# Optimization experiments

Hardware: AMD Instinct MI355X
Metric: run time of the kernel (lower is better)

## Reference

```python
import jax, jax.numpy as jnp
import numpy as np

B, L, D_MODEL = 2, 1024, 512
N_LAYERS, D_STATE, D_CONV = 6, 16, 4
D_INNER = 2 * D_MODEL          # Mamba default expand=2
DT_RANK = (D_MODEL + 15) // 16  # ceil(d_model/16) = 32
EPS = 1.1920929e-07             # torch RMSNorm default eps (fp32 machine eps)


def rmsnorm(x, w):
    return x * jax.lax.rsqrt(jnp.mean(x * x, axis=-1, keepdims=True) + EPS) * w


def selective_scan(u, dt, A, Bm, Cm, Dv):
    # u, dt: (B,L,E); A: (E,N); Bm, Cm: (B,L,N); Dv: (E,)
    dA = jnp.exp(jnp.einsum('ble,en->blen', dt, A))    # discretized A (ZOH)
    dBu = jnp.einsum('ble,bln->blen', dt * u, Bm)      # discretized B * u (Euler)

    def step(h, inp):
        dA_t, dBu_t, C_t = inp
        h = dA_t * h + dBu_t                           # (B,E,N) state update
        y = jnp.einsum('ben,bn->be', h, C_t)
        return h, y

    h0 = jnp.zeros((u.shape[0], u.shape[2], A.shape[1]), u.dtype)
    _, ys = jax.lax.scan(step, h0,
                         (dA.transpose(1, 0, 2, 3), dBu.transpose(1, 0, 2, 3),
                          Cm.transpose(1, 0, 2)))
    return ys.transpose(1, 0, 2) + u * Dv


def mamba_block(x, p):
    xz = jnp.einsum('bld,ed->ble', x, p['in_proj_w'])  # (B,L,2E)
    xi, z = jnp.split(xz, 2, axis=-1)
    # causal depthwise conv1d (kernel D_CONV) + bias + SiLU
    xc = jnp.pad(xi.transpose(0, 2, 1), ((0, 0), (0, 0), (D_CONV - 1, 0)))
    xc = jax.lax.conv_general_dilated(xc, p['conv_w'][:, None, :], (1,), 'VALID',
                                      feature_group_count=D_INNER)
    xi = jax.nn.silu(xc.transpose(0, 2, 1) + p['conv_b'])
    dbc = jnp.einsum('ble,re->blr', xi, p['x_proj_w'])  # (B,L,R+2N)
    dt, Bm, Cm = jnp.split(dbc, [DT_RANK, DT_RANK + D_STATE], axis=-1)
    dt = jax.nn.softplus(jnp.einsum('blr,er->ble', dt, p['dt_w']) + p['dt_b'])
    y = selective_scan(xi, dt, -jnp.exp(p['A_log']), Bm, Cm, p['D'])
    y = y * jax.nn.silu(z)                              # gate branch
    return jnp.einsum('ble,de->bld', y, p['out_w'])


def setup_inputs() -> dict:
    key = jax.random.key(0)
    ks = jax.random.split(key, 8)
    s = 0.02
    return {
        'x': jax.random.normal(ks[0], (B, L, D_MODEL), jnp.float32),
        'position_embedding': jax.random.normal(ks[1], (B, L, D_MODEL), jnp.float32) * 0.02,
        'norm_w': jnp.ones((D_MODEL,), jnp.float32),
        'in_proj_w': jax.random.normal(ks[2], (N_LAYERS, 2 * D_INNER, D_MODEL), jnp.float32) * s,
        'conv_w': jax.random.normal(ks[3], (N_LAYERS, D_INNER, D_CONV), jnp.float32) * 0.2,
        'conv_b': jnp.zeros((N_LAYERS, D_INNER), jnp.float32),
        'x_proj_w': jax.random.normal(ks[4], (N_LAYERS, DT_RANK + 2 * D_STATE, D_INNER), jnp.float32) * s,
        'dt_w': jax.random.normal(ks[5], (N_LAYERS, D_INNER, DT_RANK), jnp.float32) * s,
        'dt_b': jnp.full((N_LAYERS, D_INNER), -4.6, jnp.float32),  # softplus(dt_b) ~ 0.01
        'A_log': jnp.broadcast_to(
            jnp.log(jnp.arange(1, D_STATE + 1, dtype=jnp.float32)),
            (N_LAYERS, D_INNER, D_STATE)) + jnp.zeros((N_LAYERS, D_INNER, D_STATE), jnp.float32),
        'D': jnp.ones((N_LAYERS, D_INNER), jnp.float32),
        'out_w': jax.random.normal(ks[6], (N_LAYERS, D_MODEL, D_INNER), jnp.float32) * s,
    }


def reference(x, position_embedding, norm_w, in_proj_w, conv_w, conv_b,
              x_proj_w, dt_w, dt_b, A_log, D, out_w):
    stacked = dict(in_proj_w=in_proj_w, conv_w=conv_w, conv_b=conv_b,
                   x_proj_w=x_proj_w, dt_w=dt_w, dt_b=dt_b,
                   A_log=A_log, D=D, out_w=out_w)

    def body(h, p):
        h = h + position_embedding          # added at the start of every layer
        h = mamba_block(rmsnorm(h, norm_w), p)  # NOTE: no residual, per source
        return h, None

    h, _ = jax.lax.scan(body, x, stacked)
    return h
```

## Files before the change

kernel.cpp:

```cpp
#include <hip/hip_runtime.h>
#include <hip/hip_bf16.h>


typedef __attribute__((ext_vector_type(8))) short bf16x8;
typedef __attribute__((ext_vector_type(4))) float f32x4;

__device__ __forceinline__ float bf2f(unsigned short u) {
    unsigned int x = ((unsigned int)u) << 16;
    return __builtin_bit_cast(float, x);
}
__device__ __forceinline__ unsigned short f2bf(float f) {
    __hip_bfloat16 h = __float2bfloat16(f);
    return __builtin_bit_cast(unsigned short, h);
}
__device__ __forceinline__ float ldin(const void* p, size_t i, int isbf) {
    return isbf ? bf2f(((const unsigned short*)p)[i]) : ((const float*)p)[i];
}
__device__ __forceinline__ float softplus_f(float x) {
    return (x > 20.f) ? x : log1pf(__expf(x));
}
__device__ __forceinline__ void split2(float x, unsigned short& h, unsigned short& l) {
    h = f2bf(x);
    l = f2bf(x - bf2f(h));
}

#define S1 (6*2048*512)
#define S2 (6*512*1024)
#define S3 (6*64*1024)
#define S4 (6*1024*32)
#define S5 (6*1024*16)
#define S6 (6*4*1024)
#define S7 (6*1024)
__global__ __launch_bounds__(256) void wsplit_all(
    const void* __restrict__ ipw, const void* __restrict__ ow,
    const void* __restrict__ xpw, const void* __restrict__ dtw,
    const void* __restrict__ alog, const void* __restrict__ cw,
    const void* __restrict__ cb, const void* __restrict__ Dw,
    unsigned short* __restrict__ h1, unsigned short* __restrict__ l1,
    unsigned short* __restrict__ h2, unsigned short* __restrict__ l2,
    unsigned short* __restrict__ h3, unsigned short* __restrict__ l3,
    float* __restrict__ dtwT, float* __restrict__ AenT,
    float* __restrict__ cwT, float* __restrict__ cbF,
    int* __restrict__ flag)
{
    int g = blockIdx.x * 256 + threadIdx.x;
    const int isbf = (*(const unsigned int*)Dw == 0x3F800000u) ? 0 : 1;
    if (g == 0) *flag = isbf;
    if (g < S1 + S2 + S3) {
        const void* src; unsigned short *dh, *dl; int i;
        if (g < S1)            { src = ipw; dh = h1; dl = l1; i = g; }
        else if (g < S1 + S2)  { src = ow;  dh = h2; dl = l2; i = g - S1; }
        else                   { src = xpw; dh = h3; dl = l3; i = g - S1 - S2; }
        unsigned short hh, ll;
        split2(ldin(src, i, isbf), hh, ll);
        dh[i] = hh; dl[i] = ll;
    } else if (g < S1 + S2 + S3 + S4) {
        int i = g - (S1 + S2 + S3);
        int l = i >> 15, rem = i & 32767;
        int e = rem >> 5, k = rem & 31;
        dtwT[(size_t)l * 32768 + k * 1024 + e] =
            ldin(dtw, (size_t)l * 32768 + e * 32 + k, isbf);
    } else if (g < S1 + S2 + S3 + S4 + S5) {
        int i = g - (S1 + S2 + S3 + S4);
        int l = i >> 14, rem = i & 16383;
        int n = rem >> 10, e = rem & 1023;
        AenT[(size_t)l * 16384 + n * 1024 + e] =
            -__expf(ldin(alog, (size_t)l * 16384 + e * 16 + n, isbf));
    } else if (g < S1 + S2 + S3 + S4 + S5 + S6) {
        int i = g - (S1 + S2 + S3 + S4 + S5);
        int l = i >> 12, rem = i & 4095;
        int k = rem >> 10, e = rem & 1023;
        cwT[(size_t)l * 4096 + k * 1024 + e] =
            ldin(cw, (size_t)l * 4096 + e * 4 + k, isbf);
    } else if (g < S1 + S2 + S3 + S4 + S5 + S6 + S7) {
        int i = g - (S1 + S2 + S3 + S4 + S5 + S6);
        cbF[i] = ldin(cb, i, isbf);
    }
}

__global__ __launch_bounds__(512) void gemm128(
    const unsigned short* __restrict__ Ah, const unsigned short* __restrict__ Al,
    int lda,
    const unsigned short* __restrict__ Wh, const unsigned short* __restrict__ Wl,
    long woff,
    float* __restrict__ Cf, int N, int K)
{
    __shared__ __align__(16) unsigned short As[2][128][40];
    __shared__ __align__(16) unsigned short Ws[2][128][40];

    const int bid = blockIdx.x;
    const int xcd = bid & 7, s = bid >> 3;
    const int mt = (xcd >> 1) * 4 + (s & 3);
    const int nt = (xcd & 1) * 8 + (s >> 2);
    const int m0 = mt * 128, n0 = nt * 128;

    const int t = threadIdx.x, lane = t & 63, wave = t >> 6;
    const int wm = (wave & 1) * 64, wn = (wave >> 1) * 32;
    const int srow = t >> 2, scol = (t & 3) * 8;

    const unsigned short* ah = Ah + (size_t)(m0 + srow) * lda + scol;
    const unsigned short* al = Al + (size_t)(m0 + srow) * lda + scol;
    const unsigned short* wh = Wh + woff + (size_t)(n0 + srow) * K + scol;
    const unsigned short* wl = Wl + woff + (size_t)(n0 + srow) * K + scol;

    f32x4 acc[4][2] = {};
    const int fm = lane & 15, fk = (lane >> 4) * 8;

    uint4 r0, r1, r2, r3;
#define LD128(K0) do { \
        r0 = *(const uint4*)(ah + (K0)); \
        r1 = *(const uint4*)(al + (K0)); \
        r2 = *(const uint4*)(wh + (K0)); \
        r3 = *(const uint4*)(wl + (K0)); \
    } while (0)
#define ST128() do { \
        *(uint4*)(&As[0][srow][scol]) = r0; \
        *(uint4*)(&As[1][srow][scol]) = r1; \
        *(uint4*)(&Ws[0][srow][scol]) = r2; \
        *(uint4*)(&Ws[1][srow][scol]) = r3; \
    } while (0)

    LD128(0);
    ST128();
    __syncthreads();

    for (int k0 = 0; k0 < K; k0 += 32) {
        const int more = (k0 + 32 < K);
        if (more) LD128(k0 + 32);

        bf16x8 a_h[4], a_l[4], w_h[2], w_l[2];
#pragma unroll
        for (int i = 0; i < 4; ++i) {
            a_h[i] = *(const bf16x8*)(&As[0][wm + i * 16 + fm][fk]);
            a_l[i] = *(const bf16x8*)(&As[1][wm + i * 16 + fm][fk]);
        }
#pragma unroll
        for (int j = 0; j < 2; ++j) {
            w_h[j] = *(const bf16x8*)(&Ws[0][wn + j * 16 + fm][fk]);
            w_l[j] = *(const bf16x8*)(&Ws[1][wn + j * 16 + fm][fk]);
        }
#pragma unroll
        for (int mi = 0; mi < 4; ++mi)
#pragma unroll
            for (int ni = 0; ni < 2; ++ni) {
                acc[mi][ni] = __builtin_amdgcn_mfma_f32_16x16x32_bf16(
                    a_h[mi], w_h[ni], acc[mi][ni], 0, 0, 0);
                acc[mi][ni] = __builtin_amdgcn_mfma_f32_16x16x32_bf16(
                    a_h[mi], w_l[ni], acc[mi][ni], 0, 0, 0);
                acc[mi][ni] = __builtin_amdgcn_mfma_f32_16x16x32_bf16(
                    a_l[mi], w_h[ni], acc[mi][ni], 0, 0, 0);
            }

        if (more) {
            __syncthreads();
            ST128();
            __syncthreads();
        }
    }
#undef LD128
#undef ST128

    const int col = lane & 15, rb = (lane >> 4) * 4;
#pragma unroll
    for (int mi = 0; mi < 4; ++mi)
#pragma unroll
        for (int ni = 0; ni < 2; ++ni)
#pragma unroll
            for (int r = 0; r < 4; ++r) {
                int gm = m0 + wm + mi * 16 + rb + r;
                int gn = n0 + wn + ni * 16 + col;
                Cf[(size_t)gm * N + gn] = acc[mi][ni][r];
            }
}

template <int ACT, int SWZ>
__global__ __launch_bounds__(512) void gemm_hl(
    const unsigned short* __restrict__ Ah, const unsigned short* __restrict__ Al,
    int lda,
    const unsigned short* __restrict__ Wh, const unsigned short* __restrict__ Wl,
    long woff,
    float* __restrict__ Cf, long zstride,
    const void* __restrict__ bias, long boff, const int* __restrict__ flag,
    int N, int K, int Kc)
{
    const int isbf = *flag;
    __shared__ __align__(16) unsigned short As[2][2][64][40];
    __shared__ __align__(16) unsigned short Ws[2][2][64][40];

    int m0, n0, kb;
    if (SWZ) {
        const int bid = blockIdx.x;
        const int xcd = bid & 7, s = bid >> 3;
        m0 = (xcd * 4 + (s & 3)) * 64;
        n0 = (s >> 2) * 64;
        kb = 0;
    } else {
        m0 = blockIdx.x * 64; n0 = blockIdx.y * 64; kb = blockIdx.z * Kc;
    }
    const int t = threadIdx.x;
    const int lane = t & 63, wave = t >> 6;
    const int wm = (wave & 1) * 32, wn = (wave >> 1) * 16;
    const int u = t & 255;
    const int srow = u >> 2, scol = (u & 3) * 8;
    const int isA = (t < 256);

    const unsigned short* ph = isA ? (Ah + (size_t)(m0 + srow) * lda + scol)
                                   : (Wh + woff + (size_t)(n0 + srow) * K + scol);
    const unsigned short* pl = isA ? (Al + (size_t)(m0 + srow) * lda + scol)
                                   : (Wl + woff + (size_t)(n0 + srow) * K + scol);

    f32x4 acc[2] = {};

    uint4 r0, r1;
#define LD64(K0) do { \
        r0 = *(const uint4*)(ph + (K0)); \
        r1 = *(const uint4*)(pl + (K0)); \
    } while (0)
#define ST64(B) do { \
        if (isA) { \
            *(uint4*)(&As[B][0][srow][scol]) = r0; \
            *(uint4*)(&As[B][1][srow][scol]) = r1; \
        } else { \
            *(uint4*)(&Ws[B][0][srow][scol]) = r0; \
            *(uint4*)(&Ws[B][1][srow][scol]) = r1; \
        } \
    } while (0)

    LD64(kb);
    ST64(0);
    __syncthreads();

    int cur = 0;
    for (int k0 = kb; k0 < kb + Kc; k0 += 32) {
        const int more = (k0 + 32 < kb + Kc);
        if (more) LD64(k0 + 32);

        const int fm = lane & 15, fk = (lane >> 4) * 8;
        bf16x8 a0h = *(const bf16x8*)(&As[cur][0][wm + fm][fk]);
        bf16x8 a1h = *(const bf16x8*)(&As[cur][0][wm + 16 + fm][fk]);
        bf16x8 a0l = *(const bf16x8*)(&As[cur][1][wm + fm][fk]);
        bf16x8 a1l = *(const bf16x8*)(&As[cur][1][wm + 16 + fm][fk]);
        bf16x8 w0h = *(const bf16x8*)(&Ws[cur][0][wn + fm][fk]);
        bf16x8 w0l = *(const bf16x8*)(&Ws[cur][1][wn + fm][fk]);

        acc[0] = __builtin_amdgcn_mfma_f32_16x16x32_bf16(a0h, w0h, acc[0], 0, 0, 0);
        acc[1] = __builtin_amdgcn_mfma_f32_16x16x32_bf16(a1h, w0h, acc[1], 0, 0, 0);
        acc[0] = __builtin_amdgcn_mfma_f32_16x16x32_bf16(a0h, w0l, acc[0], 0, 0, 0);
        acc[1] = __builtin_amdgcn_mfma_f32_16x16x32_bf16(a1h, w0l, acc[1], 0, 0, 0);
        acc[0] = __builtin_amdgcn_mfma_f32_16x16x32_bf16(a0l, w0h, acc[0], 0, 0, 0);
        acc[1] = __builtin_amdgcn_mfma_f32_16x16x32_bf16(a1l, w0h, acc[1], 0, 0, 0);

        if (more) {
            ST64(cur ^ 1);
            __syncthreads();
            cur ^= 1;
        }
    }
#undef LD64
#undef ST64

    float* Cp = Cf + (size_t)blockIdx.z * zstride;
    const int col = lane & 15, rb = (lane >> 4) * 4;
#pragma unroll
    for (int mi = 0; mi < 2; ++mi)
#pragma unroll
        for (int r = 0; r < 4; ++r) {
            int gm = m0 + wm + mi * 16 + rb + r;
            int gn = n0 + wn + col;
            float v = acc[mi][r];
            if (bias) v += ldin(bias, boff + gn, isbf);
            if (ACT == 1) v = softplus_f(v);
            Cp[(size_t)gm * N + gn] = v;
        }
}

__global__ __launch_bounds__(256) void rmsnorm_k(
    const void* __restrict__ hsrc, int hdyn, const void* __restrict__ pos,
    const void* __restrict__ nw, const int* __restrict__ flag,
    unsigned short* __restrict__ xnh, unsigned short* __restrict__ xnl)
{
    const int isbf = *flag;
    const int row = blockIdx.x;
    const int t = threadIdx.x;
    const size_t base = (size_t)row * 512;
    float h0 = hdyn ? ldin(hsrc, base + t, isbf)       : ((const float*)hsrc)[base + t];
    float h1 = hdyn ? ldin(hsrc, base + 256 + t, isbf) : ((const float*)hsrc)[base + 256 + t];
    float v0 = h0 + ldin(pos, base + t, isbf);
    float v1 = h1 + ldin(pos, base + 256 + t, isbf);
    float ss = v0 * v0 + v1 * v1;
#pragma unroll
    for (int o = 32; o; o >>= 1) ss += __shfl_xor(ss, o, 64);
    __shared__ float sw[4];
    if ((t & 63) == 0) sw[t >> 6] = ss;
    __syncthreads();
    float tot = sw[0] + sw[1] + sw[2] + sw[3];
    float sc = rsqrtf(tot * (1.0f / 512.0f) + 1.1920929e-07f);
    float o0 = v0 * sc * ldin(nw, t, isbf);
    float o1 = v1 * sc * ldin(nw, 256 + t, isbf);
    unsigned short hh, ll;
    split2(o0, hh, ll); xnh[base + t] = hh;       xnl[base + t] = ll;
    split2(o1, hh, ll); xnh[base + 256 + t] = hh; xnl[base + 256 + t] = ll;
}

__global__ __launch_bounds__(256) void conv_silu_k(
    const float* __restrict__ xz,
    const float* __restrict__ cwT, long cwoff,
    const float* __restrict__ cbF, long cboff,
    float* __restrict__ xi,
    unsigned short* __restrict__ xih, unsigned short* __restrict__ xil)
{
    int g = blockIdx.x * 256 + threadIdx.x;
    int e = g & 1023;
    int l = (g >> 10) & 1023;
    int b = g >> 20;
    float acc = cbF[cboff + e];
#pragma unroll
    for (int k = 0; k < 4; ++k) {
        int ls = l - 3 + k;
        if (ls >= 0)
            acc += cwT[cwoff + k * 1024 + e] *
                   xz[((size_t)(b * 1024 + ls)) * 2048 + e];
    }
    acc = acc / (1.f + __expf(-acc));
    xi[g] = acc;
    unsigned short hh, ll;
    split2(acc, hh, ll);
    xih[g] = hh; xil[g] = ll;
}

#define CL 16
#define NCH 64

__global__ __launch_bounds__(256, 1) void xp_dt_scan1(
    const float* __restrict__ Pxp,
    const float* __restrict__ dtwT, long dtwoff,
    const void* __restrict__ dtb, long dtboff,
    const float* __restrict__ AenT, long aoff,
    const float* __restrict__ xi,
    const int* __restrict__ flag,
    float* __restrict__ dbc, float* __restrict__ dtf,
    float* __restrict__ S, float* __restrict__ Dsum)
{
    const int isbf = *flag;
    const int tid = threadIdx.x;
    const int c = blockIdx.x, eg = blockIdx.y, b = blockIdx.z;
    const int t0 = b * 1024 + c * CL;

    __shared__ float red[CL][64];

    for (int idx = tid; idx < CL * 64; idx += 256) {
        int ti = idx >> 6, n = idx & 63;
        float s = 0.f;
#pragma unroll
        for (int z = 0; z < 8; ++z)
            s += Pxp[(size_t)z * 131072 + (size_t)(t0 + ti) * 64 + n];
        red[ti][n] = s;
        if (eg == 0) dbc[(size_t)(t0 + ti) * 64 + n] = s;
    }

    const int e = eg * 256 + tid;

    float wk[32];
#pragma unroll
    for (int k = 0; k < 32; ++k) wk[k] = dtwT[dtwoff + (size_t)k * 1024 + e];
    const float bias = ldin(dtb, dtboff + e, isbf);
    float Aen[16];
#pragma unroll
    for (int n = 0; n < 16; ++n) Aen[n] = AenT[aoff + (size_t)n * 1024 + e];
    float uv[CL];
#pragma unroll
    for (int i = 0; i < CL; ++i) uv[i] = xi[(size_t)(t0 + i) * 1024 + e];

    __syncthreads();

    float Sn[16];
#pragma unroll
    for (int n = 0; n < 16; ++n) Sn[n] = 0.f;
    float ds = 0.f;
#pragma unroll
    for (int i = 0; i < CL; ++i) {
        const float4* rp = (const float4*)&red[i][0];
        float acc = bias;
#pragma unroll
        for (int k4 = 0; k4 < 8; ++k4) {
            float4 r4 = rp[k4];
            acc += r4.x * wk[k4 * 4 + 0] + r4.y * wk[k4 * 4 + 1]
                 + r4.z * wk[k4 * 4 + 2] + r4.w * wk[k4 * 4 + 3];
        }
        float d = softplus_f(acc);
        dtf[(size_t)(t0 + i) * 1024 + e] = d;
        ds += d;
        float du = d * uv[i];
        const float4* Bp = (const float4*)&red[i][32];
        float4 b0 = Bp[0], b1 = Bp[1], b2 = Bp[2], b3 = Bp[3];
        float Bt[16] = {b0.x,b0.y,b0.z,b0.w, b1.x,b1.y,b1.z,b1.w,
                        b2.x,b2.y,b2.z,b2.w, b3.x,b3.y,b3.z,b3.w};
#pragma unroll
        for (int n = 0; n < 16; ++n) {
            float a = __expf(d * Aen[n]);
            Sn[n] = a * Sn[n] + du * Bt[n];
        }
    }
    size_t ob = ((size_t)(b * NCH + c) * 16) * 1024 + e;
#pragma unroll
    for (int n = 0; n < 16; ++n) S[ob + (size_t)n * 1024] = Sn[n];
    Dsum[(size_t)(b * NCH + c) * 1024 + e] = ds;
}

__global__ __launch_bounds__(256, 1) void scan_stage2(
    const float* __restrict__ S, const float* __restrict__ Dsum,
    const float* __restrict__ AenT, long aoff,
    float* __restrict__ H0)
{
    int g = blockIdx.x * 256 + threadIdx.x;
    int e = g & 1023, n = (g >> 10) & 15, b = g >> 14;
    const float Aen = AenT[aoff + (size_t)n * 1024 + e];
    float H = 0.f;
    for (int cb = 0; cb < NCH; cb += 8) {
        float s[8], pj[8];
#pragma unroll
        for (int j = 0; j < 8; ++j) {
            size_t idx = ((size_t)(b * NCH + cb + j) * 16 + n) * 1024 + e;
            s[j] = S[idx];
            pj[j] = __expf(Dsum[(size_t)(b * NCH + cb + j) * 1024 + e] * Aen);
        }
#pragma unroll
        for (int j = 0; j < 8; ++j) {
            size_t idx = ((size_t)(b * NCH + cb + j) * 16 + n) * 1024 + e;
            H0[idx] = H;
            H = pj[j] * H + s[j];
        }
    }
}

__global__ __launch_bounds__(256, 1) void scan_stage3(
    const float* __restrict__ dtp, const float* __restrict__ u,
    const float* __restrict__ dbc,
    const float* __restrict__ AenT, long aoff,
    const void* __restrict__ Dv, long doff,
    const int* __restrict__ flag,
    const float* __restrict__ xz, const float* __restrict__ H0,
    unsigned short* __restrict__ yh, unsigned short* __restrict__ yl)
{
    const int isbf = *flag;
    int g = blockIdx.x * 256 + threadIdx.x;
    int e = g & 1023, c = (g >> 10) & (NCH - 1), b = g >> 16;
    int t0 = b * 1024 + c * CL;

    float dv[CL], uv[CL], zv[CL];
#pragma unroll
    for (int i = 0; i < CL; ++i) {
        dv[i] = dtp[(size_t)(t0 + i) * 1024 + e];
        uv[i] = u[(size_t)(t0 + i) * 1024 + e];
        zv[i] = xz[(size_t)(t0 + i) * 2048 + 1024 + e];
    }

    float Aen[16], h[16];
    size_t ob = ((size_t)(b * NCH + c) * 16) * 1024 + e;
#pragma unroll
    for (int n = 0; n < 16; ++n) {
        Aen[n] = AenT[aoff + (size_t)n * 1024 + e];
        h[n] = H0[ob + (size_t)n * 1024];
    }
    float De = ldin(Dv, doff + e, isbf);
#pragma unroll
    for (int i = 0; i < CL; ++i) {
        float d = dv[i], uu = uv[i], du = d * uu;
        const float4* Bp = (const float4*)(dbc + (size_t)(t0 + i) * 64 + 32);
        float4 b0 = Bp[0], b1 = Bp[1], b2 = Bp[2], b3 = Bp[3];
        float4 c0 = Bp[4], c1 = Bp[5], c2 = Bp[6], c3 = Bp[7];
        float Bt[16] = {b0.x,b0.y,b0.z,b0.w, b1.x,b1.y,b1.z,b1.w,
                        b2.x,b2.y,b2.z,b2.w, b3.x,b3.y,b3.z,b3.w};
        float Ct[16] = {c0.x,c0.y,c0.z,c0.w, c1.x,c1.y,c1.z,c1.w,
                        c2.x,c2.y,c2.z,c2.w, c3.x,c3.y,c3.z,c3.w};
        float y = 0.f;
#pragma unroll
        for (int n = 0; n < 16; ++n) {
            float a = __expf(d * Aen[n]);
            h[n] = a * h[n] + du * Bt[n];
            y += h[n] * Ct[n];
        }
        float sz = zv[i] / (1.f + __expf(-zv[i]));
        float yv = (y + uu * De) * sz;
        unsigned short hh, ll;
        split2(yv, hh, ll);
        yh[(size_t)(t0 + i) * 1024 + e] = hh;
        yl[(size_t)(t0 + i) * 1024 + e] = ll;
    }
}

extern "C" void kernel_launch(void* const* d_in, const int* in_sizes, int n_in,
                              void* d_out, int out_size, void* d_ws, size_t ws_size,
                              hipStream_t stream)
{
    const void* x    = d_in[0];
    const void* pos  = d_in[1];
    const void* nw   = d_in[2];
    const void* ipw  = d_in[3];
    const void* cw   = d_in[4];
    const void* cb   = d_in[5];
    const void* xpw  = d_in[6];
    const void* dtw  = d_in[7];
    const void* dtb  = d_in[8];
    const void* alog = d_in[9];
    const void* Dw   = d_in[10];
    const void* ow   = d_in[11];

    char* w = (char*)d_ws;
    auto take = [&](size_t bytes) { char* p = w; w += (bytes + 255) & ~255ull; return p; };

    float* h    = (float*)take(2048ull * 512 * 4);
    float* xz   = (float*)take(2048ull * 2048 * 4);
    float* xi   = (float*)take(2048ull * 1024 * 4);
    float* dtf  = (float*)take(2048ull * 1024 * 4);
    float* dbc  = (float*)take(2048ull * 64 * 4);
    float* S    = (float*)take(2ull * NCH * 16 * 1024 * 4);
    float* H0   = (float*)take(2ull * NCH * 16 * 1024 * 4);
    float* Dsum = (float*)take(2ull * NCH * 1024 * 4);
    float* Pxp  = (float*)take(8ull * 2048 * 64 * 4);
    float* dtwT = (float*)take(6ull * 32 * 1024 * 4);
    float* AenT = (float*)take(6ull * 16 * 1024 * 4);
    float* cwT  = (float*)take(6ull * 4 * 1024 * 4);
    float* cbF  = (float*)take(6ull * 1024 * 4);
    unsigned short* xnh = (unsigned short*)take(2048ull * 512 * 2);
    unsigned short* xnl = (unsigned short*)take(2048ull * 512 * 2);
    unsigned short* xih = (unsigned short*)take(2048ull * 1024 * 2);
    unsigned short* xil = (unsigned short*)take(2048ull * 1024 * 2);
    unsigned short* yh  = (unsigned short*)take(2048ull * 1024 * 2);
    unsigned short* yl  = (unsigned short*)take(2048ull * 1024 * 2);
    unsigned short* wip_h = (unsigned short*)take(6ull * 2048 * 512 * 2);
    unsigned short* wip_l = (unsigned short*)take(6ull * 2048 * 512 * 2);
    unsigned short* wow_h = (unsigned short*)take(6ull * 512 * 1024 * 2);
    unsigned short* wow_l = (unsigned short*)take(6ull * 512 * 1024 * 2);
    unsigned short* wxp_h = (unsigned short*)take(6ull * 64 * 1024 * 2);
    unsigned short* wxp_l = (unsigned short*)take(6ull * 64 * 1024 * 2);
    int* flag = (int*)take(256);

    wsplit_all<<<(S1 + S2 + S3 + S4 + S5 + S6 + S7 + 255) / 256, 256, 0, stream>>>(
        ipw, ow, xpw, dtw, alog, cw, cb, Dw,
        wip_h, wip_l, wow_h, wow_l, wxp_h, wxp_l, dtwT, AenT, cwT, cbF, flag);

    for (int l = 0; l < 6; ++l) {
        rmsnorm_k<<<2048, 256, 0, stream>>>(
            l == 0 ? x : (const void*)h, l == 0 ? 1 : 0, pos, nw, flag, xnh, xnl);
        gemm128<<<256, 512, 0, stream>>>(
            xnh, xnl, 512, wip_h, wip_l, (long)l * 2048 * 512, xz, 2048, 512);
        conv_silu_k<<<8192, 256, 0, stream>>>(xz, cwT, (long)l * 4096, cbF, (long)l * 1024,
                                              xi, xih, xil);
        gemm_hl<0, 0><<<dim3(32, 1, 8), 512, 0, stream>>>(
            xih, xil, 1024, wxp_h, wxp_l, (long)l * 64 * 1024,
            Pxp, 2048l * 64, nullptr, 0, flag, 64, 1024, 128);
        xp_dt_scan1<<<dim3(NCH, 4, 2), 256, 0, stream>>>(
            Pxp, dtwT, (long)l * 32768, dtb, (long)l * 1024,
            AenT, (long)l * 16384, xi, flag, dbc, dtf, S, Dsum);
        scan_stage2<<<128, 256, 0, stream>>>(S, Dsum, AenT, (long)l * 16384, H0);
        scan_stage3<<<512, 256, 0, stream>>>(dtf, xi, dbc, AenT, (long)l * 16384,
                                             Dw, (long)l * 1024, flag, xz, H0, yh, yl);
        float* outp = (l < 5) ? h : (float*)d_out;
        gemm_hl<0, 1><<<256, 512, 0, stream>>>(
            yh, yl, 1024, wow_h, wow_l, (long)l * 512 * 1024,
            outp, 0, nullptr, 0, flag, 512, 1024, 1024);
    }
}
```

Measured before the change: 758.3 us.

## Fuse causal conv+SiLU into x_proj GEMM and recompute dt in scan stage3

Replaces the separate conv_silu kernel and x_proj GEMM with one kernel that computes the depthwise conv, SiLU and bf16 hi/lo split while staging the A tile into shared memory. This removes the xih/xil intermediate buffers and one launch. It also stops writing the dt buffer in scan stage1; stage3 recomputes the dt projection and softplus from dbc instead of reading dt back. In exchange, each conv output is now computed only once, inside the x_proj split whose K-slice covers it, and stage3 loads 32 extra weights per thread and does more arithmetic.

```diff
diff --git a/kernel.cpp b/kernel.cpp
--- a/kernel.cpp
+++ b/kernel.cpp
@@ -173,6 +173,149 @@
             }
 }
 
+__global__ __launch_bounds__(512) void conv_xproj(
+    const float* __restrict__ xz,
+    const float* __restrict__ cwT, long cwoff,
+    const float* __restrict__ cbF, long cboff,
+    const unsigned short* __restrict__ Wh, const unsigned short* __restrict__ Wl,
+    long woff,
+    float* __restrict__ Pxp, long zstride,
+    float* __restrict__ xi,
+    int K, int Kc)
+{
+    __shared__ __align__(16) unsigned short As[2][2][64][40];
+    __shared__ __align__(16) unsigned short Ws[2][2][64][40];
+    __shared__ float cwL[4][128];
+    __shared__ float cbL[128];
+
+    const int m0 = blockIdx.x * 64;
+    const int z  = blockIdx.z;
+    const int kb = z * Kc;
+    const int t = threadIdx.x;
+    const int lane = t & 63, wave = t >> 6;
+    const int wm = (wave & 1) * 32, wn = (wave >> 1) * 16;
+    const int u = t & 255;
+    const int srow = u >> 2, scol = (u & 3) * 8;
+    const int isA = (t < 256);
+
+    if (t < 512) {
+        int k = t >> 7, el = t & 127;
+        cwL[k][el] = cwT[cwoff + (size_t)k * 1024 + kb + el];
+    }
+    if (t < 128) cbL[t] = cbF[cboff + kb + t];
+
+    const int gr = m0 + srow;
+    const int brow = gr >> 10, lrow = gr & 1023;
+
+    const unsigned short* wh = Wh + woff + (size_t)srow * K + scol;
+    const unsigned short* wl = Wl + woff + (size_t)srow * K + scol;
+
+    f32x4 acc[2] = {};
+    float xr[4][8];
+    uint4 r0, r1;
+
+    auto LDA = [&](int K0) {
+        int ee = K0 + scol;
+#pragma unroll
+        for (int k = 0; k < 4; ++k) {
+            int ls = lrow - 3 + k;
+            int lsc = ls < 0 ? 0 : ls;
+            const float* p = xz + ((size_t)(brow * 1024 + lsc)) * 2048 + ee;
+            float4 q0 = *(const float4*)p;
+            float4 q1 = *(const float4*)(p + 4);
+            xr[k][0] = q0.x; xr[k][1] = q0.y; xr[k][2] = q0.z; xr[k][3] = q0.w;
+            xr[k][4] = q1.x; xr[k][5] = q1.y; xr[k][6] = q1.z; xr[k][7] = q1.w;
+        }
+    };
+    auto STA = [&](int B, int K0) {
+        int ee = K0 + scol, el = ee - kb;
+        float a[8];
+#pragma unroll
+        for (int j = 0; j < 8; ++j) a[j] = cbL[el + j];
+#pragma unroll
+        for (int k = 0; k < 4; ++k) {
+            if (lrow - 3 + k >= 0) {
+#pragma unroll
+                for (int j = 0; j < 8; ++j)
+                    a[j] += cwL[k][el + j] * xr[k][j];
+            }
+        }
+#pragma unroll
+        for (int j = 0; j < 8; ++j) a[j] = a[j] / (1.f + __expf(-a[j]));
+        float4 o0, o1;
+        o0.x = a[0]; o0.y = a[1]; o0.z = a[2]; o0.w = a[3];
+        o1.x = a[4]; o1.y = a[5]; o1.z = a[6]; o1.w = a[7];
+        *(float4*)&xi[(size_t)gr * 1024 + ee]     = o0;
+        *(float4*)&xi[(size_t)gr * 1024 + ee + 4] = o1;
+        unsigned short hv[8], lv[8];
+#pragma unroll
+        for (int j = 0; j < 8; ++j) split2(a[j], hv[j], lv[j]);
+        uint4 HV, LV;
+        HV.x = (unsigned)hv[0] | ((unsigned)hv[1] << 16);
+        HV.y = (unsigned)hv[2] | ((unsigned)hv[3] << 16);
+        HV.z = (unsigned)hv[4] | ((unsigned)hv[5] << 16);
+        HV.w = (unsigned)hv[6] | ((unsigned)hv[7] << 16);
+        LV.x = (unsigned)lv[0] | ((unsigned)lv[1] << 16);
+        LV.y = (unsigned)lv[2] | ((unsigned)lv[3] << 16);
+        LV.z = (unsigned)lv[4] | ((unsigned)lv[5] << 16);
+        LV.w = (unsigned)lv[6] | ((unsigned)lv[7] << 16);
+        *(uint4*)&As[B][0][srow][scol] = HV;
+        *(uint4*)&As[B][1][srow][scol] = LV;
+    };
+    auto LDW = [&](int K0) {
+        r0 = *(const uint4*)(wh + K0);
+        r1 = *(const uint4*)(wl + K0);
+    };
+    auto STW = [&](int B) {
+        *(uint4*)(&Ws[B][0][srow][scol]) = r0;
+        *(uint4*)(&Ws[B][1][srow][scol]) = r1;
+    };
+
+    __syncthreads();
+
+    if (isA) LDA(kb); else LDW(kb);
+    if (isA) STA(0, kb); else STW(0);
+    __syncthreads();
+
+    int cur = 0;
+    for (int k0 = kb; k0 < kb + Kc; k0 += 32) {
+        const int more = (k0 + 32 < kb + Kc);
+        if (more) { if (isA) LDA(k0 + 32); else LDW(k0 + 32); }
+
+        const int fm = lane & 15, fk = (lane >> 4) * 8;
+        bf16x8 a0h = *(const bf16x8*)(&As[cur][0][wm + fm][fk]);
+        bf16x8 a1h = *(const bf16x8*)(&As[cur][0][wm + 16 + fm][fk]);
+        bf16x8 a0l = *(const bf16x8*)(&As[cur][1][wm + fm][fk]);
+        bf16x8 a1l = *(const bf16x8*)(&As[cur][1][wm + 16 + fm][fk]);
+        bf16x8 w0h = *(const bf16x8*)(&Ws[cur][0][wn + fm][fk]);
+        bf16x8 w0l = *(const bf16x8*)(&Ws[cur][1][wn + fm][fk]);
+
+        acc[0] = __builtin_amdgcn_mfma_f32_16x16x32_bf16(a0h, w0h, acc[0], 0, 0, 0);
+        acc[1] = __builtin_amdgcn_mfma_f32_16x16x32_bf16(a1h, w0h, acc[1], 0, 0, 0);
+        acc[0] = __builtin_amdgcn_mfma_f32_16x16x32_bf16(a0h, w0l, acc[0], 0, 0, 0);
+        acc[1] = __builtin_amdgcn_mfma_f32_16x16x32_bf16(a1h, w0l, acc[1], 0, 0, 0);
+        acc[0] = __builtin_amdgcn_mfma_f32_16x16x32_bf16(a0l, w0h, acc[0], 0, 0, 0);
+        acc[1] = __builtin_amdgcn_mfma_f32_16x16x32_bf16(a1l, w0h, acc[1], 0, 0, 0);
+
+        if (more) {
+            if (isA) STA(cur ^ 1, k0 + 32); else STW(cur ^ 1);
+            __syncthreads();
+            cur ^= 1;
+        }
+    }
+
+    float* Cp = Pxp + (size_t)z * zstride;
+    const int col = lane & 15, rb = (lane >> 4) * 4;
+#pragma unroll
+    for (int mi = 0; mi < 2; ++mi)
+#pragma unroll
+        for (int r = 0; r < 4; ++r) {
+            int gm = m0 + wm + mi * 16 + rb + r;
+            int gn = wn + col;
+            Cp[(size_t)gm * 64 + gn] = acc[mi][r];
+        }
+}
+
 template <int ACT, int SWZ>
 __global__ __launch_bounds__(512) void gemm_hl(
     const unsigned short* __restrict__ Ah, const unsigned short* __restrict__ Al,
@@ -302,32 +445,6 @@
     split2(o1, hh, ll); xnh[base + 256 + t] = hh; xnl[base + 256 + t] = ll;
 }
 
-__global__ __launch_bounds__(256) void conv_silu_k(
-    const float* __restrict__ xz,
-    const float* __restrict__ cwT, long cwoff,
-    const float* __restrict__ cbF, long cboff,
-    float* __restrict__ xi,
-    unsigned short* __restrict__ xih, unsigned short* __restrict__ xil)
-{
-    int g = blockIdx.x * 256 + threadIdx.x;
-    int e = g & 1023;
-    int l = (g >> 10) & 1023;
-    int b = g >> 20;
-    float acc = cbF[cboff + e];
-#pragma unroll
-    for (int k = 0; k < 4; ++k) {
-        int ls = l - 3 + k;
-        if (ls >= 0)
-            acc += cwT[cwoff + k * 1024 + e] *
-                   xz[((size_t)(b * 1024 + ls)) * 2048 + e];
-    }
-    acc = acc / (1.f + __expf(-acc));
-    xi[g] = acc;
-    unsigned short hh, ll;
-    split2(acc, hh, ll);
-    xih[g] = hh; xil[g] = ll;
-}
-
 #define CL 16
 #define NCH 64
 
@@ -338,7 +455,7 @@
     const float* __restrict__ AenT, long aoff,
     const float* __restrict__ xi,
     const int* __restrict__ flag,
-    float* __restrict__ dbc, float* __restrict__ dtf,
+    float* __restrict__ dbc,
     float* __restrict__ S, float* __restrict__ Dsum)
 {
     const int isbf = *flag;
@@ -388,7 +505,6 @@
                  + r4.z * wk[k4 * 4 + 2] + r4.w * wk[k4 * 4 + 3];
         }
         float d = softplus_f(acc);
-        dtf[(size_t)(t0 + i) * 1024 + e] = d;
         ds += d;
         float du = d * uv[i];
         const float4* Bp = (const float4*)&red[i][32];
@@ -434,7 +550,9 @@
 }
 
 __global__ __launch_bounds__(256, 1) void scan_stage3(
-    const float* __restrict__ dtp, const float* __restrict__ u,
+    const float* __restrict__ dtwT, long dtwoff,
+    const void* __restrict__ dtb, long dtboff,
+    const float* __restrict__ u,
     const float* __restrict__ dbc,
     const float* __restrict__ AenT, long aoff,
     const void* __restrict__ Dv, long doff,
@@ -447,10 +565,14 @@
     int e = g & 1023, c = (g >> 10) & (NCH - 1), b = g >> 16;
     int t0 = b * 1024 + c * CL;
 
-    float dv[CL], uv[CL], zv[CL];
+    float wk[32];
+#pragma unroll
+    for (int k = 0; k < 32; ++k) wk[k] = dtwT[dtwoff + (size_t)k * 1024 + e];
+    const float bias = ldin(dtb, dtboff + e, isbf);
+
+    float uv[CL], zv[CL];
 #pragma unroll
     for (int i = 0; i < CL; ++i) {
-        dv[i] = dtp[(size_t)(t0 + i) * 1024 + e];
         uv[i] = u[(size_t)(t0 + i) * 1024 + e];
         zv[i] = xz[(size_t)(t0 + i) * 2048 + 1024 + e];
     }
@@ -465,8 +587,17 @@
     float De = ldin(Dv, doff + e, isbf);
 #pragma unroll
     for (int i = 0; i < CL; ++i) {
-        float d = dv[i], uu = uv[i], du = d * uu;
-        const float4* Bp = (const float4*)(dbc + (size_t)(t0 + i) * 64 + 32);
+        const float4* rp = (const float4*)(dbc + (size_t)(t0 + i) * 64);
+        float accd = bias;
+#pragma unroll
+        for (int k4 = 0; k4 < 8; ++k4) {
+            float4 r4 = rp[k4];
+            accd += r4.x * wk[k4 * 4 + 0] + r4.y * wk[k4 * 4 + 1]
+                  + r4.z * wk[k4 * 4 + 2] + r4.w * wk[k4 * 4 + 3];
+        }
+        float d = softplus_f(accd);
+        float uu = uv[i], du = d * uu;
+        const float4* Bp = rp + 8;
         float4 b0 = Bp[0], b1 = Bp[1], b2 = Bp[2], b3 = Bp[3];
         float4 c0 = Bp[4], c1 = Bp[5], c2 = Bp[6], c3 = Bp[7];
         float Bt[16] = {b0.x,b0.y,b0.z,b0.w, b1.x,b1.y,b1.z,b1.w,
@@ -512,7 +643,6 @@
     float* h    = (float*)take(2048ull * 512 * 4);
     float* xz   = (float*)take(2048ull * 2048 * 4);
     float* xi   = (float*)take(2048ull * 1024 * 4);
-    float* dtf  = (float*)take(2048ull * 1024 * 4);
     float* dbc  = (float*)take(2048ull * 64 * 4);
     float* S    = (float*)take(2ull * NCH * 16 * 1024 * 4);
     float* H0   = (float*)take(2ull * NCH * 16 * 1024 * 4);
@@ -524,8 +654,6 @@
     float* cbF  = (float*)take(6ull * 1024 * 4);
     unsigned short* xnh = (unsigned short*)take(2048ull * 512 * 2);
     unsigned short* xnl = (unsigned short*)take(2048ull * 512 * 2);
-    unsigned short* xih = (unsigned short*)take(2048ull * 1024 * 2);
-    unsigned short* xil = (unsigned short*)take(2048ull * 1024 * 2);
     unsigned short* yh  = (unsigned short*)take(2048ull * 1024 * 2);
     unsigned short* yl  = (unsigned short*)take(2048ull * 1024 * 2);
     unsigned short* wip_h = (unsigned short*)take(6ull * 2048 * 512 * 2);
@@ -545,17 +673,18 @@
             l == 0 ? x : (const void*)h, l == 0 ? 1 : 0, pos, nw, flag, xnh, xnl);
         gemm128<<<256, 512, 0, stream>>>(
             xnh, xnl, 512, wip_h, wip_l, (long)l * 2048 * 512, xz, 2048, 512);
-        conv_silu_k<<<8192, 256, 0, stream>>>(xz, cwT, (long)l * 4096, cbF, (long)l * 1024,
-                                              xi, xih, xil);
-        gemm_hl<0, 0><<<dim3(32, 1, 8), 512, 0, stream>>>(
-            xih, xil, 1024, wxp_h, wxp_l, (long)l * 64 * 1024,
-            Pxp, 2048l * 64, nullptr, 0, flag, 64, 1024, 128);
+        conv_xproj<<<dim3(32, 1, 8), 512, 0, stream>>>(
+            xz, cwT, (long)l * 4096, cbF, (long)l * 1024,
+            wxp_h, wxp_l, (long)l * 64 * 1024,
+            Pxp, 2048l * 64, xi, 1024, 128);
         xp_dt_scan1<<<dim3(NCH, 4, 2), 256, 0, stream>>>(
             Pxp, dtwT, (long)l * 32768, dtb, (long)l * 1024,
-            AenT, (long)l * 16384, xi, flag, dbc, dtf, S, Dsum);
+            AenT, (long)l * 16384, xi, flag, dbc, S, Dsum);
         scan_stage2<<<128, 256, 0, stream>>>(S, Dsum, AenT, (long)l * 16384, H0);
-        scan_stage3<<<512, 256, 0, stream>>>(dtf, xi, dbc, AenT, (long)l * 16384,
-                                             Dw, (long)l * 1024, flag, xz, H0, yh, yl);
+        scan_stage3<<<512, 256, 0, stream>>>(
+            dtwT, (long)l * 32768, dtb, (long)l * 1024,
+            xi, dbc, AenT, (long)l * 16384,
+            Dw, (long)l * 1024, flag, xz, H0, yh, yl);
         float* outp = (l < 5) ? h : (float*)d_out;
         gemm_hl<0, 1><<<256, 512, 0, stream>>>(
             yh, yl, 1024, wow_h, wow_l, (long)l * 512 * 1024,
```

After: 798.2 us. 5.3% more time.

## Fuse three scan stages into one persistent kernel with grid barriers

Applied to the files above, without the earlier changes.

Merges the chunk-local scan, the inter-chunk prefix and the output pass into a single 512-block kernel that uses atomic-counter grid barriers. dt, u and the B/C values stay in registers and shared memory instead of round-tripping through global dtf/dbc buffers, and two kernel launches per layer go away. The design assumes all 512 blocks are co-resident (launch_bounds 256,2 on 256 CUs) and otherwise deadlocks. Spin-waiting adds barrier latency, and only 128 blocks do work during the middle phase.

```diff
diff --git a/kernel.cpp b/kernel.cpp
--- a/kernel.cpp
+++ b/kernel.cpp
@@ -22,6 +22,18 @@
 __device__ __forceinline__ void split2(float x, unsigned short& h, unsigned short& l) {
     h = f2bf(x);
     l = f2bf(x - bf2f(h));
+}
+
+__device__ __forceinline__ void gsync(int* cnt, int target) {
+    __syncthreads();
+    __threadfence();
+    if (threadIdx.x == 0) {
+        __hip_atomic_fetch_add(cnt, 1, __ATOMIC_ACQ_REL, __HIP_MEMORY_SCOPE_AGENT);
+        while (__hip_atomic_load(cnt, __ATOMIC_ACQUIRE, __HIP_MEMORY_SCOPE_AGENT) < target)
+            __builtin_amdgcn_s_sleep(2);
+    }
+    __syncthreads();
+    __threadfence();
 }
 
 #define S1 (6*2048*512)
@@ -331,19 +343,27 @@
 #define CL 16
 #define NCH 64
 
-__global__ __launch_bounds__(256, 1) void xp_dt_scan1(
-    const float* __restrict__ Pxp,
-    const float* __restrict__ dtwT, long dtwoff,
-    const void* __restrict__ dtb, long dtboff,
-    const float* __restrict__ AenT, long aoff,
-    const float* __restrict__ xi,
-    const int* __restrict__ flag,
-    float* __restrict__ dbc, float* __restrict__ dtf,
-    float* __restrict__ S, float* __restrict__ Dsum)
-{
-    const int isbf = *flag;
+struct ScanP {
+    const float* Pxp;
+    const float* dtwT; long dtwoff;
+    const void* dtb;  long dtboff;
+    const float* AenT; long aoff;
+    const float* xi;
+    const float* xz;
+    const void* Dv;   long doff;
+    const int* flag;
+    float* S; float* Dsum; float* H0;
+    unsigned short* yh; unsigned short* yl;
+    int* bar; int ep0;
+};
+
+__global__ __launch_bounds__(256, 2) void scan_all(ScanP p)
+{
+    const int isbf = *p.flag;
     const int tid = threadIdx.x;
-    const int c = blockIdx.x, eg = blockIdx.y, b = blockIdx.z;
+    const int bid = blockIdx.x;
+    const int eg = bid & 3, c = (bid >> 2) & 63, b = bid >> 8;
+    const int e = eg * 256 + tid;
     const int t0 = b * 1024 + c * CL;
 
     __shared__ float red[CL][64];
@@ -353,26 +373,24 @@
         float s = 0.f;
 #pragma unroll
         for (int z = 0; z < 8; ++z)
-            s += Pxp[(size_t)z * 131072 + (size_t)(t0 + ti) * 64 + n];
+            s += p.Pxp[(size_t)z * 131072 + (size_t)(t0 + ti) * 64 + n];
         red[ti][n] = s;
-        if (eg == 0) dbc[(size_t)(t0 + ti) * 64 + n] = s;
-    }
-
-    const int e = eg * 256 + tid;
+    }
 
     float wk[32];
 #pragma unroll
-    for (int k = 0; k < 32; ++k) wk[k] = dtwT[dtwoff + (size_t)k * 1024 + e];
-    const float bias = ldin(dtb, dtboff + e, isbf);
+    for (int k = 0; k < 32; ++k) wk[k] = p.dtwT[p.dtwoff + (size_t)k * 1024 + e];
+    const float bias = ldin(p.dtb, p.dtboff + e, isbf);
     float Aen[16];
 #pragma unroll
-    for (int n = 0; n < 16; ++n) Aen[n] = AenT[aoff + (size_t)n * 1024 + e];
+    for (int n = 0; n < 16; ++n) Aen[n] = p.AenT[p.aoff + (size_t)n * 1024 + e];
     float uv[CL];
 #pragma unroll
-    for (int i = 0; i < CL; ++i) uv[i] = xi[(size_t)(t0 + i) * 1024 + e];
+    for (int i = 0; i < CL; ++i) uv[i] = p.xi[(size_t)(t0 + i) * 1024 + e];
 
     __syncthreads();
 
+    float dv[CL];
     float Sn[16];
 #pragma unroll
     for (int n = 0; n < 16; ++n) Sn[n] = 0.f;
@@ -388,7 +406,7 @@
                  + r4.z * wk[k4 * 4 + 2] + r4.w * wk[k4 * 4 + 3];
         }
         float d = softplus_f(acc);
-        dtf[(size_t)(t0 + i) * 1024 + e] = d;
+        dv[i] = d;
         ds += d;
         float du = d * uv[i];
         const float4* Bp = (const float4*)&red[i][32];
@@ -403,70 +421,47 @@
     }
     size_t ob = ((size_t)(b * NCH + c) * 16) * 1024 + e;
 #pragma unroll
-    for (int n = 0; n < 16; ++n) S[ob + (size_t)n * 1024] = Sn[n];
-    Dsum[(size_t)(b * NCH + c) * 1024 + e] = ds;
-}
-
-__global__ __launch_bounds__(256, 1) void scan_stage2(
-    const float* __restrict__ S, const float* __restrict__ Dsum,
-    const float* __restrict__ AenT, long aoff,
-    float* __restrict__ H0)
-{
-    int g = blockIdx.x * 256 + threadIdx.x;
-    int e = g & 1023, n = (g >> 10) & 15, b = g >> 14;
-    const float Aen = AenT[aoff + (size_t)n * 1024 + e];
-    float H = 0.f;
-    for (int cb = 0; cb < NCH; cb += 8) {
-        float s[8], pj[8];
-#pragma unroll
-        for (int j = 0; j < 8; ++j) {
-            size_t idx = ((size_t)(b * NCH + cb + j) * 16 + n) * 1024 + e;
-            s[j] = S[idx];
-            pj[j] = __expf(Dsum[(size_t)(b * NCH + cb + j) * 1024 + e] * Aen);
-        }
-#pragma unroll
-        for (int j = 0; j < 8; ++j) {
-            size_t idx = ((size_t)(b * NCH + cb + j) * 16 + n) * 1024 + e;
-            H0[idx] = H;
-            H = pj[j] * H + s[j];
-        }
-    }
-}
-
-__global__ __launch_bounds__(256, 1) void scan_stage3(
-    const float* __restrict__ dtp, const float* __restrict__ u,
-    const float* __restrict__ dbc,
-    const float* __restrict__ AenT, long aoff,
-    const void* __restrict__ Dv, long doff,
-    const int* __restrict__ flag,
-    const float* __restrict__ xz, const float* __restrict__ H0,
-    unsigned short* __restrict__ yh, unsigned short* __restrict__ yl)
-{
-    const int isbf = *flag;
-    int g = blockIdx.x * 256 + threadIdx.x;
-    int e = g & 1023, c = (g >> 10) & (NCH - 1), b = g >> 16;
-    int t0 = b * 1024 + c * CL;
-
-    float dv[CL], uv[CL], zv[CL];
-#pragma unroll
-    for (int i = 0; i < CL; ++i) {
-        dv[i] = dtp[(size_t)(t0 + i) * 1024 + e];
-        uv[i] = u[(size_t)(t0 + i) * 1024 + e];
-        zv[i] = xz[(size_t)(t0 + i) * 2048 + 1024 + e];
-    }
-
-    float Aen[16], h[16];
-    size_t ob = ((size_t)(b * NCH + c) * 16) * 1024 + e;
-#pragma unroll
-    for (int n = 0; n < 16; ++n) {
-        Aen[n] = AenT[aoff + (size_t)n * 1024 + e];
-        h[n] = H0[ob + (size_t)n * 1024];
-    }
-    float De = ldin(Dv, doff + e, isbf);
+    for (int n = 0; n < 16; ++n) p.S[ob + (size_t)n * 1024] = Sn[n];
+    p.Dsum[(size_t)(b * NCH + c) * 1024 + e] = ds;
+
+    gsync(p.bar, (p.ep0 + 1) * 512);
+
+    if (bid < 128) {
+        int g = bid * 256 + tid;
+        int e2 = g & 1023, n2 = (g >> 10) & 15, b2 = g >> 14;
+        const float Aen2 = p.AenT[p.aoff + (size_t)n2 * 1024 + e2];
+        float H = 0.f;
+        for (int cb = 0; cb < NCH; cb += 8) {
+            float s[8], pj[8];
+#pragma unroll
+            for (int j = 0; j < 8; ++j) {
+                size_t idx = ((size_t)(b2 * NCH + cb + j) * 16 + n2) * 1024 + e2;
+                s[j] = p.S[idx];
+                pj[j] = __expf(p.Dsum[(size_t)(b2 * NCH + cb + j) * 1024 + e2] * Aen2);
+            }
+#pragma unroll
+            for (int j = 0; j < 8; ++j) {
+                size_t idx = ((size_t)(b2 * NCH + cb + j) * 16 + n2) * 1024 + e2;
+                p.H0[idx] = H;
+                H = pj[j] * H + s[j];
+            }
+        }
+    }
+
+    gsync(p.bar, (p.ep0 + 2) * 512);
+
+    float zv[CL];
+#pragma unroll
+    for (int i = 0; i < CL; ++i)
+        zv[i] = p.xz[(size_t)(t0 + i) * 2048 + 1024 + e];
+    float hS[16];
+#pragma unroll
+    for (int n = 0; n < 16; ++n) hS[n] = p.H0[ob + (size_t)n * 1024];
+    float De = ldin(p.Dv, p.doff + e, isbf);
 #pragma unroll
     for (int i = 0; i < CL; ++i) {
         float d = dv[i], uu = uv[i], du = d * uu;
-        const float4* Bp = (const float4*)(dbc + (size_t)(t0 + i) * 64 + 32);
+        const float4* Bp = (const float4*)&red[i][32];
         float4 b0 = Bp[0], b1 = Bp[1], b2 = Bp[2], b3 = Bp[3];
         float4 c0 = Bp[4], c1 = Bp[5], c2 = Bp[6], c3 = Bp[7];
         float Bt[16] = {b0.x,b0.y,b0.z,b0.w, b1.x,b1.y,b1.z,b1.w,
@@ -477,17 +472,19 @@
 #pragma unroll
         for (int n = 0; n < 16; ++n) {
             float a = __expf(d * Aen[n]);
-            h[n] = a * h[n] + du * Bt[n];
-            y += h[n] * Ct[n];
+            hS[n] = a * hS[n] + du * Bt[n];
+            y += hS[n] * Ct[n];
         }
         float sz = zv[i] / (1.f + __expf(-zv[i]));
         float yv = (y + uu * De) * sz;
         unsigned short hh, ll;
         split2(yv, hh, ll);
-        yh[(size_t)(t0 + i) * 1024 + e] = hh;
-        yl[(size_t)(t0 + i) * 1024 + e] = ll;
-    }
-}
+        p.yh[(size_t)(t0 + i) * 1024 + e] = hh;
+        p.yl[(size_t)(t0 + i) * 1024 + e] = ll;
+    }
+}
+
+__global__ void init_bar(int* bar) { *bar = 0; }
 
 extern "C" void kernel_launch(void* const* d_in, const int* in_sizes, int n_in,
                               void* d_out, int out_size, void* d_ws, size_t ws_size,
@@ -512,8 +509,6 @@
     float* h    = (float*)take(2048ull * 512 * 4);
     float* xz   = (float*)take(2048ull * 2048 * 4);
     float* xi   = (float*)take(2048ull * 1024 * 4);
-    float* dtf  = (float*)take(2048ull * 1024 * 4);
-    float* dbc  = (float*)take(2048ull * 64 * 4);
     float* S    = (float*)take(2ull * NCH * 16 * 1024 * 4);
     float* H0   = (float*)take(2ull * NCH * 16 * 1024 * 4);
     float* Dsum = (float*)take(2ull * NCH * 1024 * 4);
@@ -535,7 +530,9 @@
     unsigned short* wxp_h = (unsigned short*)take(6ull * 64 * 1024 * 2);
     unsigned short* wxp_l = (unsigned short*)take(6ull * 64 * 1024 * 2);
     int* flag = (int*)take(256);
-
+    int* bar  = (int*)take(256);
+
+    init_bar<<<1, 1, 0, stream>>>(bar);
     wsplit_all<<<(S1 + S2 + S3 + S4 + S5 + S6 + S7 + 255) / 256, 256, 0, stream>>>(
         ipw, ow, xpw, dtw, alog, cw, cb, Dw,
         wip_h, wip_l, wow_h, wow_l, wxp_h, wxp_l, dtwT, AenT, cwT, cbF, flag);
@@ -550,12 +547,18 @@
         gemm_hl<0, 0><<<dim3(32, 1, 8), 512, 0, stream>>>(
             xih, xil, 1024, wxp_h, wxp_l, (long)l * 64 * 1024,
             Pxp, 2048l * 64, nullptr, 0, flag, 64, 1024, 128);
-        xp_dt_scan1<<<dim3(NCH, 4, 2), 256, 0, stream>>>(
-            Pxp, dtwT, (long)l * 32768, dtb, (long)l * 1024,
-            AenT, (long)l * 16384, xi, flag, dbc, dtf, S, Dsum);
-        scan_stage2<<<128, 256, 0, stream>>>(S, Dsum, AenT, (long)l * 16384, H0);
-        scan_stage3<<<512, 256, 0, stream>>>(dtf, xi, dbc, AenT, (long)l * 16384,
-                                             Dw, (long)l * 1024, flag, xz, H0, yh, yl);
+        ScanP sp;
+        sp.Pxp = Pxp;
+        sp.dtwT = dtwT; sp.dtwoff = (long)l * 32768;
+        sp.dtb = dtb;   sp.dtboff = (long)l * 1024;
+        sp.AenT = AenT; sp.aoff = (long)l * 16384;
+        sp.xi = xi; sp.xz = xz;
+        sp.Dv = Dw; sp.doff = (long)l * 1024;
+        sp.flag = flag;
+        sp.S = S; sp.Dsum = Dsum; sp.H0 = H0;
+        sp.yh = yh; sp.yl = yl;
+        sp.bar = bar; sp.ep0 = 2 * l;
+        scan_all<<<512, 256, 0, stream>>>(sp);
         float* outp = (l < 5) ? h : (float*)d_out;
         gemm_hl<0, 1><<<256, 512, 0, stream>>>(
             yh, yl, 1024, wow_h, wow_l, (long)l * 512 * 1024,
```

New measurement: 2.847 ms. 275% more time.
